# Performance work log

Measured on AMD Instinct MI355X. Metric: run time of the kernel, lower is better.

## Reference

```python
import jax, jax.numpy as jnp
import numpy as np

N = 100000
E = 1200000
NFEAT = 64
NCLASS = 64


def setup_inputs() -> dict:
    key = jax.random.key(0)
    k1, k2, k3, k4, k5, k6 = jax.random.split(key, 6)
    x = jax.random.normal(k1, (N, NFEAT), dtype=jnp.float32)
    edge_row = jax.random.randint(k2, (E,), 0, N, dtype=jnp.int32).astype(jnp.int64)
    edge_col = jax.random.randint(k3, (E,), 0, N, dtype=jnp.int32).astype(jnp.int64)
    edge_weight = jax.random.uniform(k4, (E,), dtype=jnp.float32)
    W = jax.random.normal(k5, (NCLASS, NFEAT), dtype=jnp.float32) / np.sqrt(NFEAT)
    b = jax.random.normal(k6, (NCLASS,), dtype=jnp.float32) * 0.01
    return {"x": x, "edge_row": edge_row, "edge_col": edge_col,
            "edge_weight": edge_weight, "W": W, "b": b, "k": 2}


def _spmm(edge_row, edge_col, edge_weight, x):
    # out[i] = sum_{e: row[e]==i} w[e] * x[col[e]]  == (sparse adj) @ x
    msgs = edge_weight[:, None] * x[edge_col]          # [E, F]
    return jax.ops.segment_sum(msgs, edge_row, num_segments=N)


def reference(x, edge_row, edge_col, edge_weight, W, b, k):
    h = x
    for _ in range(k):  # k is a small static int (propagation depth)
        h = _spmm(edge_row, edge_col, edge_weight, h)
    return h @ W.T + b  # nn.Linear(nfeat, nclass)
```

## Files before the change

kernel.cpp:

```cpp
#include <hip/hip_runtime.h>
#include <hip/hip_fp16.h>

#define FF 64
#define RPB 128
#define RCAP 2048
#define PAIRCAP 2432
#define PCHUNK 4096
#define NBCNT 782

typedef _Float16 f16x8 __attribute__((ext_vector_type(8)));
typedef float    f32x4 __attribute__((ext_vector_type(4)));


union HU { unsigned int u; __half2 h; };

__device__ __forceinline__ unsigned int f2h2(float a, float b) {
    HU t; t.h = __floats2half2_rn(a, b);
    return t.u;
}
__device__ __forceinline__ __half2 u2h2(unsigned int u) {
    HU t; t.u = u;
    return t.h;
}


__global__ void cvt_and_partition(const float* __restrict__ x, unsigned short* __restrict__ xh,
                                  int nelem,
                                  const int* __restrict__ erow, const int* __restrict__ ecol,
                                  const float* __restrict__ ew, int* __restrict__ bcursor,
                                  uint2* __restrict__ bent, int E, int partBlocks) {
    __shared__ int lcnt[NBCNT];
    __shared__ int lbase[NBCNT];
    int t = threadIdx.x;

    if ((int)blockIdx.x >= partBlocks) {
        int i = ((blockIdx.x - partBlocks) * 256 + t) * 4;
        if (i < nelem) {
            float4 v = *(const float4*)&x[i];
            uint2 st;
            st.x = f2h2(v.x, v.y);
            st.y = f2h2(v.z, v.w);
            *(uint2*)&xh[i] = st;
        }
        return;
    }

    for (int i = t; i < NBCNT; i += 256) lcnt[i] = 0;
    __syncthreads();

    int base = blockIdx.x * PCHUNK;
    int lim  = min(PCHUNK, E - base);

    for (int i = t; i < lim; i += 256)
        atomicAdd(&lcnt[erow[base + i] >> 7], 1);
    __syncthreads();
    for (int i = t; i < NBCNT; i += 256) {
        int c = lcnt[i];
        lbase[i] = c ? atomicAdd(&bcursor[i], c) : 0;
        lcnt[i] = 0;
    }
    __syncthreads();
    for (int i = t; i < lim; i += 256) {
        int e = base + i;
        int r = erow[e];
        int bkt = r >> 7;
        int off = atomicAdd(&lcnt[bkt], 1);
        uint2 en;
        en.x = ((unsigned)(r & (RPB - 1)) << 17) | (unsigned)ecol[e];
        en.y = (unsigned)__float_as_int(ew[e]);
        bent[(size_t)bkt * RCAP + lbase[bkt] + off] = en;
    }
}


__device__ __forceinline__ void build_lds_csr_g(const uint2* __restrict__ src, int cnt,
                                                int2* pairLds, int* deg, int* pofs,
                                                int* cur, int* part, int t, int nthr) {
    if (t < RPB) { deg[t] = 0; cur[t] = 0; }
    __syncthreads();
    for (int i = t; i < cnt; i += nthr)
        atomicAdd(&deg[src[i].x >> 17], 1);
    __syncthreads();

    if (t < RPB) part[t] = (deg[t] + 3) & ~3;
    __syncthreads();
    for (int off = 1; off < RPB; off <<= 1) {
        int add = (t < RPB && t >= off) ? part[t - off] : 0;
        __syncthreads();
        if (t < RPB) part[t] += add;
        __syncthreads();
    }
    if (t < RPB) pofs[t] = part[t] - ((deg[t] + 3) & ~3);
    __syncthreads();

    for (int i = t; i < cnt; i += nthr) {
        uint2 e = src[i];
        int lr  = e.x >> 17;
        int col = e.x & 0x1FFFF;
        float w = __int_as_float((int)e.y);
        int pos = pofs[lr] + atomicAdd(&cur[lr], 1);
        pairLds[pos] = make_int2(col, (int)f2h2(w, w));
    }
    if (t < RPB) {
        int a = deg[t], p = (a + 3) & ~3;
        for (int q = a; q < p; ++q) pairLds[pofs[t] + q] = make_int2(0, 0);
    }
    __syncthreads();
}


__device__ __forceinline__ void pkfma4(__half2 w2, uint4 v, __half2 acc[4]) {
    acc[0] = __hfma2(w2, u2h2(v.x), acc[0]);
    acc[1] = __hfma2(w2, u2h2(v.y), acc[1]);
    acc[2] = __hfma2(w2, u2h2(v.z), acc[2]);
    acc[3] = __hfma2(w2, u2h2(v.w), acc[3]);
}

__device__ __forceinline__ void row_accum8_lds(const int4* __restrict__ p, int n4,
                                               const uint4* __restrict__ hin4,
                                               int lg, __half2 acc[4]) {
    if (n4 <= 0) return;
    int4 q0 = p[0];
    int4 q1 = p[1];
    uint4 v0 = hin4[(size_t)q0.x * 8 + lg];
    uint4 v1 = hin4[(size_t)q0.z * 8 + lg];
    uint4 v2 = hin4[(size_t)q1.x * 8 + lg];
    uint4 v3 = hin4[(size_t)q1.z * 8 + lg];
    for (int i = 2; i < n4; i += 2) {
        int4 r0 = p[i];
        int4 r1 = p[i + 1];
        uint4 u0 = hin4[(size_t)r0.x * 8 + lg];
        uint4 u1 = hin4[(size_t)r0.z * 8 + lg];
        uint4 u2 = hin4[(size_t)r1.x * 8 + lg];
        uint4 u3 = hin4[(size_t)r1.z * 8 + lg];
        pkfma4(u2h2((unsigned)q0.y), v0, acc);
        pkfma4(u2h2((unsigned)q0.w), v1, acc);
        pkfma4(u2h2((unsigned)q1.y), v2, acc);
        pkfma4(u2h2((unsigned)q1.w), v3, acc);
        q0 = r0; q1 = r1;
        v0 = u0; v1 = u1; v2 = u2; v3 = u3;
    }
    pkfma4(u2h2((unsigned)q0.y), v0, acc);
    pkfma4(u2h2((unsigned)q0.w), v1, acc);
    pkfma4(u2h2((unsigned)q1.y), v2, acc);
    pkfma4(u2h2((unsigned)q1.w), v3, acc);
}


__global__ __launch_bounds__(512) void spmm1(const uint2* __restrict__ bent,
        const int* __restrict__ bcount, const unsigned short* __restrict__ hin,
        unsigned short* __restrict__ hout, int Nn) {
    __shared__ int2 pairLds[PAIRCAP];
    __shared__ int  deg[RPB], pofs[RPB], cur[RPB], part[RPB];
    const uint4* hin4 = (const uint4*)hin;
    int b = blockIdx.x, t = threadIdx.x;
    int cnt = min(bcount[b], RCAP);

    build_lds_csr_g(bent + (size_t)b * RCAP, cnt, pairLds, deg, pofs, cur, part, t, 512);

    int lane = t & 63, g = lane >> 3, lg = lane & 7;
    int rbase = (t >> 6) * 8 + g;
#pragma unroll
    for (int pass = 0; pass < 2; ++pass) {
        int rloc = pass * 64 + rbase;
        int row  = b * RPB + rloc;
        __half2 acc[4] = {__half2{0,0}, __half2{0,0}, __half2{0,0}, __half2{0,0}};
        int plen = (deg[rloc] + 3) & ~3;
        row_accum8_lds((const int4*)pairLds + (pofs[rloc] >> 1), plen >> 1, hin4, lg, acc);
        if (row < Nn)
            ((uint4*)hout)[(size_t)row * 8 + lg] = *(const uint4*)acc;
    }
}


__global__ __launch_bounds__(512) void spmm2(const uint2* __restrict__ bent,
        const int* __restrict__ bcount, const unsigned short* __restrict__ hin,
        const float* __restrict__ Wm, const float* __restrict__ bias,
        float* __restrict__ out, int Nn) {
    __shared__ int2 pairLds[PAIRCAP];
    __shared__ int  deg[RPB], pofs[RPB], cur[RPB], part[RPB];
    __shared__ unsigned short shw[64][72];
    __shared__ unsigned short shh[128][72];
    __shared__ float sbias[64];
    const uint4* hin4 = (const uint4*)hin;
    int b = blockIdx.x, t = threadIdx.x;
    int cnt = min(bcount[b], RCAP);

    for (int i = t; i < 1024; i += 512) {
        int idx = i * 4;
        int c = idx >> 6, f = idx & 63;
        float4 w4 = *(const float4*)&Wm[idx];
        uint2 pk;
        pk.x = f2h2(w4.x, w4.y);
        pk.y = f2h2(w4.z, w4.w);
        *(uint2*)&shw[c][f] = pk;
    }
    if (t < 64) sbias[t] = bias[t];

    build_lds_csr_g(bent + (size_t)b * RCAP, cnt, pairLds, deg, pofs, cur, part, t, 512);

    int lane = t & 63, g = lane >> 3, lg = lane & 7;
    int rbase = (t >> 6) * 8 + g;
#pragma unroll
    for (int pass = 0; pass < 2; ++pass) {
        int rloc = pass * 64 + rbase;
        __half2 acc[4] = {__half2{0,0}, __half2{0,0}, __half2{0,0}, __half2{0,0}};
        int plen = (deg[rloc] + 3) & ~3;
        row_accum8_lds((const int4*)pairLds + (pofs[rloc] >> 1), plen >> 1, hin4, lg, acc);
        *(uint4*)&shh[rloc][lg * 8] = *(const uint4*)acc;
    }
    __syncthreads();

    int tt = t >> 6;
    int mr = lane & 15, kg = lane >> 4;
    f32x4 c0 = {0.f,0.f,0.f,0.f}, c1 = {0.f,0.f,0.f,0.f};
    f32x4 c2 = {0.f,0.f,0.f,0.f}, c3 = {0.f,0.f,0.f,0.f};
#pragma unroll
    for (int kc = 0; kc < 2; ++kc) {
        int k0 = kc * 32 + kg * 8;
        f16x8 a  = *(const f16x8*)&shh[tt * 16 + mr][k0];
        f16x8 b0 = *(const f16x8*)&shw[mr][k0];
        f16x8 b1 = *(const f16x8*)&shw[16 + mr][k0];
        f16x8 b2 = *(const f16x8*)&shw[32 + mr][k0];
        f16x8 b3 = *(const f16x8*)&shw[48 + mr][k0];
        c0 = __builtin_amdgcn_mfma_f32_16x16x32_f16(a, b0, c0, 0, 0, 0);
        c1 = __builtin_amdgcn_mfma_f32_16x16x32_f16(a, b1, c1, 0, 0, 0);
        c2 = __builtin_amdgcn_mfma_f32_16x16x32_f16(a, b2, c2, 0, 0, 0);
        c3 = __builtin_amdgcn_mfma_f32_16x16x32_f16(a, b3, c3, 0, 0, 0);
    }
#pragma unroll
    for (int j = 0; j < 4; ++j) {
        int orow = b * RPB + tt * 16 + kg * 4 + j;
        if (orow < Nn) {
            float* op = &out[(size_t)orow * FF];
            op[mr]      = c0[j] + sbias[mr];
            op[16 + mr] = c1[j] + sbias[16 + mr];
            op[32 + mr] = c2[j] + sbias[32 + mr];
            op[48 + mr] = c3[j] + sbias[48 + mr];
        }
    }
}


extern "C" void kernel_launch(void* const* d_in, const int* in_sizes, int n_in,
                              void* d_out, int out_size, void* d_ws, size_t ws_size,
                              hipStream_t stream) {
    const float* x    = (const float*)d_in[0];
    const int*   erow = (const int*)  d_in[1];
    const int*   ecol = (const int*)  d_in[2];
    const float* ew   = (const float*)d_in[3];
    const float* W    = (const float*)d_in[4];
    const float* b    = (const float*)d_in[5];

    int E  = in_sizes[1];
    int Nn = in_sizes[0] / FF;
    int nelem = Nn * FF;
    int NB = (Nn + RPB - 1) / RPB;

    char*  ws  = (char*)d_ws;
    size_t off = 0;
    auto alloc = [&](size_t bytes) { void* p = ws + off; off += (bytes + 255) & ~255ULL; return p; };
    unsigned short* xh   = (unsigned short*)alloc((size_t)nelem * 2);
    unsigned short* h1h  = (unsigned short*)alloc((size_t)nelem * 2);
    uint2*          bent = (uint2*)alloc((size_t)NB * RCAP * sizeof(uint2));
    int*            bcursor = (int*)alloc(NBCNT * sizeof(int));

    hipMemsetAsync(bcursor, 0, NBCNT * sizeof(int), stream);

    int partBlocks = (E + PCHUNK - 1) / PCHUNK;
    int cvtBlocks  = (nelem / 4 + 255) / 256;
    cvt_and_partition<<<partBlocks + cvtBlocks, 256, 0, stream>>>(
        x, xh, nelem, erow, ecol, ew, bcursor, bent, E, partBlocks);

    spmm1<<<NB, 512, 0, stream>>>(bent, bcursor, xh, h1h, Nn);
    spmm2<<<NB, 512, 0, stream>>>(bent, bcursor, h1h, W, b, (float*)d_out, Nn);
}
```

Baseline: 98.06 us.

## Replace global atomic bucket cursors with deterministic count-scan-scatter partition

Splits the fused edge partition kernel into three steps: per-chunk bucket counts, a per-bucket prefix scan over chunks, and a scatter that uses the precomputed bases. This removes the global atomicAdd on bucket cursors and the memset, and makes bucket layout deterministic and ordered by chunk, which may improve locality in the SpMM kernels. In exchange it adds two extra kernel launches, reads erow twice, and writes and reads per-bucket, per-chunk count and base arrays.

```diff
diff --git a/kernel.cpp b/kernel.cpp
--- a/kernel.cpp
+++ b/kernel.cpp
@@ -24,13 +24,10 @@
 }
 
 
-__global__ void cvt_and_partition(const float* __restrict__ x, unsigned short* __restrict__ xh,
-                                  int nelem,
-                                  const int* __restrict__ erow, const int* __restrict__ ecol,
-                                  const float* __restrict__ ew, int* __restrict__ bcursor,
-                                  uint2* __restrict__ bent, int E, int partBlocks) {
+__global__ void cvt_and_count(const float* __restrict__ x, unsigned short* __restrict__ xh,
+                              int nelem, const int* __restrict__ erow,
+                              int* __restrict__ cnts, int E, int partBlocks) {
     __shared__ int lcnt[NBCNT];
-    __shared__ int lbase[NBCNT];
     int t = threadIdx.x;
 
     if ((int)blockIdx.x >= partBlocks) {
@@ -47,28 +44,75 @@
 
     for (int i = t; i < NBCNT; i += 256) lcnt[i] = 0;
     __syncthreads();
-
     int base = blockIdx.x * PCHUNK;
     int lim  = min(PCHUNK, E - base);
-
     for (int i = t; i < lim; i += 256)
         atomicAdd(&lcnt[erow[base + i] >> 7], 1);
     __syncthreads();
+    for (int i = t; i < NBCNT; i += 256)
+        cnts[(size_t)i * partBlocks + blockIdx.x] = lcnt[i];
+}
+
+
+__global__ void scan_bases(const int* __restrict__ cnts, int* __restrict__ bases,
+                           int* __restrict__ bcount, int nb) {
+    __shared__ int s[256];
+    int bkt = blockIdx.x, t = threadIdx.x;
+    const int* c = cnts + (size_t)bkt * nb;
+    int* bs = bases + (size_t)bkt * nb;
+
+    int v0 = (t < nb) ? c[t] : 0;
+    s[t] = v0; __syncthreads();
+    for (int off = 1; off < 256; off <<= 1) {
+        int a = (t >= off) ? s[t - off] : 0;
+        __syncthreads();
+        s[t] += a;
+        __syncthreads();
+    }
+    int ex0 = s[t] - v0;
+    int tot0 = s[255];
+    __syncthreads();
+
+    int v1 = (t + 256 < nb) ? c[t + 256] : 0;
+    s[t] = v1; __syncthreads();
+    for (int off = 1; off < 256; off <<= 1) {
+        int a = (t >= off) ? s[t - off] : 0;
+        __syncthreads();
+        s[t] += a;
+        __syncthreads();
+    }
+    int ex1 = tot0 + s[t] - v1;
+    int tot = tot0 + s[255];
+
+    if (t < nb)       bs[t]       = bkt * RCAP + ex0;
+    if (t + 256 < nb) bs[t + 256] = bkt * RCAP + ex1;
+    if (t == 0)       bcount[bkt] = tot;
+}
+
+
+__global__ void scatter(const int* __restrict__ erow, const int* __restrict__ ecol,
+                        const float* __restrict__ ew, const int* __restrict__ bases,
+                        uint2* __restrict__ bent, int E, int partBlocks) {
+    __shared__ int bas[NBCNT];
+    __shared__ int cur[NBCNT];
+    int b = blockIdx.x, t = threadIdx.x;
     for (int i = t; i < NBCNT; i += 256) {
-        int c = lcnt[i];
-        lbase[i] = c ? atomicAdd(&bcursor[i], c) : 0;
-        lcnt[i] = 0;
-    }
-    __syncthreads();
+        bas[i] = bases[(size_t)i * partBlocks + b];
+        cur[i] = 0;
+    }
+    __syncthreads();
+
+    int base = b * PCHUNK;
+    int lim  = min(PCHUNK, E - base);
     for (int i = t; i < lim; i += 256) {
         int e = base + i;
         int r = erow[e];
         int bkt = r >> 7;
-        int off = atomicAdd(&lcnt[bkt], 1);
+        int off = atomicAdd(&cur[bkt], 1);
         uint2 en;
         en.x = ((unsigned)(r & (RPB - 1)) << 17) | (unsigned)ecol[e];
         en.y = (unsigned)__float_as_int(ew[e]);
-        bent[(size_t)bkt * RCAP + lbase[bkt] + off] = en;
+        bent[bas[bkt] + off] = en;
     }
 }
 
@@ -256,6 +300,8 @@
     int Nn = in_sizes[0] / FF;
     int nelem = Nn * FF;
     int NB = (Nn + RPB - 1) / RPB;
+    int partBlocks = (E + PCHUNK - 1) / PCHUNK;
+    int cvtBlocks  = (nelem / 4 + 255) / 256;
 
     char*  ws  = (char*)d_ws;
     size_t off = 0;
@@ -263,15 +309,15 @@
     unsigned short* xh   = (unsigned short*)alloc((size_t)nelem * 2);
     unsigned short* h1h  = (unsigned short*)alloc((size_t)nelem * 2);
     uint2*          bent = (uint2*)alloc((size_t)NB * RCAP * sizeof(uint2));
-    int*            bcursor = (int*)alloc(NBCNT * sizeof(int));
-
-    hipMemsetAsync(bcursor, 0, NBCNT * sizeof(int), stream);
-
-    int partBlocks = (E + PCHUNK - 1) / PCHUNK;
-    int cvtBlocks  = (nelem / 4 + 255) / 256;
-    cvt_and_partition<<<partBlocks + cvtBlocks, 256, 0, stream>>>(
-        x, xh, nelem, erow, ecol, ew, bcursor, bent, E, partBlocks);
-
-    spmm1<<<NB, 512, 0, stream>>>(bent, bcursor, xh, h1h, Nn);
-    spmm2<<<NB, 512, 0, stream>>>(bent, bcursor, h1h, W, b, (float*)d_out, Nn);
-}
+    int* cnts   = (int*)alloc((size_t)NBCNT * partBlocks * sizeof(int));
+    int* bases  = (int*)alloc((size_t)NBCNT * partBlocks * sizeof(int));
+    int* bcount = (int*)alloc(NBCNT * sizeof(int));
+
+    cvt_and_count<<<partBlocks + cvtBlocks, 256, 0, stream>>>(
+        x, xh, nelem, erow, cnts, E, partBlocks);
+    scan_bases<<<NBCNT, 256, 0, stream>>>(cnts, bases, bcount, partBlocks);
+    scatter<<<partBlocks, 256, 0, stream>>>(erow, ecol, ew, bases, bent, E, partBlocks);
+
+    spmm1<<<NB, 512, 0, stream>>>(bent, bcount, xh, h1h, Nn);
+    spmm2<<<NB, 512, 0, stream>>>(bent, bcount, h1h, W, b, (float*)d_out, Nn);
+}
```

After: 96.16 us. No clear change (-1.9%).
